# Performance work log

Hardware: AMD Instinct MI355X
Metric: run time of the kernel (lower is better)

Reference implementation:

```python
import jax, jax.numpy as jnp
import numpy as np

IN_DIM = 256
OUT_DIM = 256
HAS_MASK = True


def setup_inputs() -> dict:
    key = jax.random.key(0)
    kx, kq, kk, kv = jax.random.split(key, 4)
    n = 8192
    x = jax.random.normal(kx, (n, IN_DIM), dtype=jnp.float32)
    # parameters (original uses torch.empty; we initialize with small randn)
    scale = 1.0 / np.sqrt(IN_DIM)
    W_query = jax.random.normal(kq, (IN_DIM, OUT_DIM), dtype=jnp.float32) * scale
    W_key = jax.random.normal(kk, (IN_DIM, OUT_DIM), dtype=jnp.float32) * scale
    W_value = jax.random.normal(kv, (IN_DIM, OUT_DIM), dtype=jnp.float32) * scale
    return {"x": x, "W_query": W_query, "W_key": W_key, "W_value": W_value}


def reference(x, W_query, W_key, W_value):
    n = x.shape[0]
    q = x @ W_query            # [n, d]
    k = x @ W_key              # [n, d]
    v = x @ W_value            # [n, d]
    sqrt_d = jnp.sqrt(jnp.asarray(OUT_DIM, dtype=jnp.float32))
    scores = (q @ k.T) / sqrt_d  # [n, n]
    if HAS_MASK:
        # torch.triu(-1e9 * ones(n, n)) keeps the diagonal -> diagonal is masked too
        mask = jnp.triu(jnp.full((n, n), -1000000000.0, dtype=jnp.float32))
        scores = scores + mask
    attn = jax.nn.softmax(scores, axis=1)  # row-wise softmax
    return attn @ v            # [n, d]
```

## Files before the change

### kernel.cpp

```cpp
#include <hip/hip_runtime.h>
#include <hip/hip_bf16.h>
#include <stdint.h>

#define DIM 256

typedef float f32x4  __attribute__((ext_vector_type(4)));
typedef float f32x16 __attribute__((ext_vector_type(16)));
typedef short bf16x8 __attribute__((ext_vector_type(8)));
typedef short bf16x4 __attribute__((ext_vector_type(4)));

__device__ __forceinline__ unsigned short f2bf(float f) {
  union { float f; uint32_t u; } v; v.f = f;
  uint32_t u = v.u;
  u += 0x7FFFu + ((u >> 16) & 1u);
  return (unsigned short)(u >> 16);
}

__device__ __forceinline__ uint32_t pack2(float lo, float hi) {
  return (uint32_t)f2bf(lo) | ((uint32_t)f2bf(hi) << 16);
}

__device__ __forceinline__ void gload16(const unsigned short* g, unsigned short* l) {
  __builtin_amdgcn_global_load_lds(
      (const __attribute__((address_space(1))) unsigned int*)g,
      (__attribute__((address_space(3))) unsigned int*)l, 16, 0, 0);
}

__global__ __launch_bounds__(256) void k_prep(const float* __restrict__ Wq,
    const float* __restrict__ Wk, const float* __restrict__ Wv,
    unsigned short* __restrict__ Wt, const float* __restrict__ x,
    float* __restrict__ partial, int n) {
  __shared__ unsigned short WL32[32][264];
  if (blockIdx.x < 24) {
    const int w  = blockIdx.x >> 3;
    const int kc = blockIdx.x & 7;
    const float* W = (w == 0) ? Wq : (w == 1) ? Wk : Wv;
    const int tid = threadIdx.x;
#pragma unroll
    for (int it = 0; it < 8; ++it) {
      const int row = it * 4 + (tid >> 6);
      const int col = (tid & 63) * 4;
      f32x4 v = *(const f32x4*)(W + (size_t)(kc * 32 + row) * DIM + col);
      bf16x4 b;
      b[0] = (short)f2bf(v[0]); b[1] = (short)f2bf(v[1]);
      b[2] = (short)f2bf(v[2]); b[3] = (short)f2bf(v[3]);
      *(bf16x4*)(&WL32[row][col]) = b;
    }
    __syncthreads();
    const int lane = tid & 63;
    const int ww = tid >> 6;
    const int g = lane >> 4, c = lane & 15;
#pragma unroll
    for (int jt = 0; jt < 4; ++jt) {
      const int nt = jt * 4 + ww;
      bf16x8 o;
#pragma unroll
      for (int j = 0; j < 8; ++j)
        o[j] = (short)WL32[g * 8 + j][nt * 16 + c];
      *(bf16x8*)(Wt + (size_t)((w * 16 + nt) * 8 + kc) * 512 + lane * 8) = o;
    }
  } else {
    const int b = blockIdx.x - 24, tid = threadIdx.x;
    float acc = 0.f;
    const float* xp = x + (size_t)b * 128 * DIM + tid;
    for (int r = 0; r < 128; ++r) acc += xp[r * DIM];
    partial[b * DIM + tid] = acc;
  }
}

__global__ __launch_bounds__(256, 2) void k_proj(const float* __restrict__ x,
    const unsigned short* __restrict__ Wt, unsigned short* __restrict__ Q,
    unsigned short* __restrict__ KS, unsigned short* __restrict__ VS, int n) {
  __shared__ unsigned short XL[64][264];
  __shared__ unsigned short WL[2][16][512];
  const int rb = blockIdx.x * 64;
  const int w = blockIdx.y;
  const int wave = threadIdx.x >> 6;
  const int lane = threadIdx.x & 63;
  const int g = lane >> 4;
  const int c = lane & 15;
  const int row0 = rb + wave * 16;

  for (int rr = 0; rr < 16; ++rr) {
    const int r = wave * 16 + rr;
    f32x4 v = *(const f32x4*)(x + (size_t)(rb + r) * DIM + lane * 4);
    bf16x4 b;
    b[0] = (short)f2bf(v[0]); b[1] = (short)f2bf(v[1]);
    b[2] = (short)f2bf(v[2]); b[3] = (short)f2bf(v[3]);
    *(bf16x4*)(&XL[r][lane * 4]) = b;
  }
  __syncthreads();

  bf16x8 af[8];
#pragma unroll
  for (int kc = 0; kc < 8; ++kc)
    af[kc] = *(const bf16x8*)(&XL[wave * 16 + c][kc * 32 + g * 8]);

  const unsigned short* Wsrc = Wt + (size_t)w * DIM * DIM + lane * 8;
  auto stagew = [&](int buf, int p) {
#pragma unroll
    for (int q2 = 0; q2 < 4; ++q2) {
      const int m = wave * 4 + q2;
      gload16(Wsrc + (size_t)(p * 16 + m) * 512, &WL[buf][m][0]);
    }
  };

  f32x4 acc[16];
#pragma unroll
  for (int t = 0; t < 16; ++t) acc[t] = (f32x4){0.f, 0.f, 0.f, 0.f};

  stagew(0, 0);
  int buf = 0;
#pragma unroll 1
  for (int p = 0; p < 8; ++p) {
    if (p < 7) {
      stagew(buf ^ 1, p + 1);
      asm volatile("s_waitcnt vmcnt(4)" ::: "memory");
    } else {
      asm volatile("s_waitcnt vmcnt(0)" ::: "memory");
    }
    __builtin_amdgcn_sched_barrier(0);
    __builtin_amdgcn_s_barrier();
    __builtin_amdgcn_sched_barrier(0);
#pragma unroll
    for (int q = 0; q < 2; ++q) {
      const int nt = p * 2 + q;
#pragma unroll
      for (int kc = 0; kc < 8; ++kc) {
        bf16x8 b = *(const bf16x8*)(&WL[buf][q * 8 + kc][lane * 8]);
        acc[nt] = __builtin_amdgcn_mfma_f32_16x16x32_bf16(af[kc], b, acc[nt], 0, 0, 0);
      }
    }
    __builtin_amdgcn_sched_barrier(0);
    __builtin_amdgcn_s_barrier();
    __builtin_amdgcn_sched_barrier(0);
    buf ^= 1;
  }

  if (w == 0) {
#pragma unroll
    for (int nt = 0; nt < 16; ++nt)
#pragma unroll
      for (int r = 0; r < 4; ++r)
        Q[(size_t)(row0 + 4 * g + r) * DIM + nt * 16 + c] = f2bf(acc[nt][r] * 0.0625f);
  } else if (w == 1) {
    const int kbase = (row0 >> 5) * 8192 + ((row0 & 31) + 4 * g) * 8 + (c & 7);
#pragma unroll
    for (int nt = 0; nt < 16; ++nt) {
      const int gb = (2 * nt + (c >> 3)) * 256;
#pragma unroll
      for (int r = 0; r < 4; ++r)
        KS[kbase + gb + r * 8] = f2bf(acc[nt][r]);
    }
  } else {
    const int j0 = row0 + 4 * g;
    unsigned short* vdst = VS + (size_t)(j0 >> 5) * 8192
                              + ((j0 >> 3) & 3) * 2048 + (j0 & 7);
#pragma unroll
    for (int nt = 0; nt < 16; ++nt) {
      const int col = nt * 16 + c;
      bf16x4 pv;
      pv[0] = (short)f2bf(acc[nt][0]); pv[1] = (short)f2bf(acc[nt][1]);
      pv[2] = (short)f2bf(acc[nt][2]); pv[3] = (short)f2bf(acc[nt][3]);
      *(bf16x4*)(vdst + col * 8) = pv;
    }
  }
}

__global__ void k_meanB(const float* __restrict__ partial, const float* __restrict__ Wv,
                        float* __restrict__ out, int n) {
  __shared__ float xm[DIM];
  const int tid = threadIdx.x;
  float acc = 0.f;
  const int nb = n / 128;
  for (int b = 0; b < nb; ++b) acc += partial[b * DIM + tid];
  xm[tid] = acc / (float)n;
  __syncthreads();
  float o = 0.f;
  for (int k = 0; k < DIM; ++k) o += xm[k] * Wv[k * DIM + tid];
  out[tid] = o;
}

__global__ __launch_bounds__(512, 4) void k_flash2(const unsigned short* __restrict__ Q,
    const unsigned short* __restrict__ KS, const unsigned short* __restrict__ VS,
    float* __restrict__ out, int n) {
  __shared__ float so[4][16][257];
  __shared__ float sml[4][2][16];
  __shared__ unsigned short plds[8][16][40];

  const int wave = threadIdx.x >> 6;
  const int lane = threadIdx.x & 63;
  const int g = lane >> 4;
  const int c = lane & 15;
  const int ntiles = n >> 4;
  const int tile = ntiles - 1 - (int)blockIdx.x;
  const int qb = tile << 4;

  bf16x8 qf[8];
  const unsigned short* qp = Q + (size_t)(qb + c) * DIM;
#pragma unroll
  for (int kc = 0; kc < 8; ++kc)
    qf[kc] = *(const bf16x8*)(qp + kc * 32 + g * 8);

  f32x4 o[16];
#pragma unroll
  for (int t = 0; t < 16; ++t) o[t] = (f32x4){0.f, 0.f, 0.f, 0.f};
  float m_r[4] = {-1e30f, -1e30f, -1e30f, -1e30f};
  float l_r[4] = {0.f, 0.f, 0.f, 0.f};

  const int nchunk = ((qb + 14) >> 5) + 1;
  for (int kt = wave; kt < nchunk; kt += 8) {
    const int k0 = kt << 5;
    const unsigned short* kch = KS + (size_t)(k0 >> 5) * 8192;
    f32x4 s0 = {0.f, 0.f, 0.f, 0.f}, s1 = {0.f, 0.f, 0.f, 0.f};
#pragma unroll
    for (int kc = 0; kc < 8; ++kc) {
      bf16x8 kb0 = *(const bf16x8*)(kch + (4 * kc + g) * 256 + c * 8);
      bf16x8 kb1 = *(const bf16x8*)(kch + (4 * kc + g) * 256 + (16 + c) * 8);
      s0 = __builtin_amdgcn_mfma_f32_16x16x32_bf16(qf[kc], kb0, s0, 0, 0, 0);
      s1 = __builtin_amdgcn_mfma_f32_16x16x32_bf16(qf[kc], kb1, s1, 0, 0, 0);
    }
    if (k0 + 31 >= qb) {
#pragma unroll
      for (int r = 0; r < 4; ++r) {
        const int qrow = qb + 4 * g + r;
        if (k0 + c >= qrow)      s0[r] = -1e9f;
        if (k0 + 16 + c >= qrow) s1[r] = -1e9f;
      }
    }
    f32x4 p0, p1;
    float alpha[4];
#pragma unroll
    for (int r = 0; r < 4; ++r) {
      float mx = fmaxf(s0[r], s1[r]);
      mx = fmaxf(mx, __shfl_xor(mx, 1, 64));
      mx = fmaxf(mx, __shfl_xor(mx, 2, 64));
      mx = fmaxf(mx, __shfl_xor(mx, 4, 64));
      mx = fmaxf(mx, __shfl_xor(mx, 8, 64));
      const float mn = fmaxf(m_r[r], mx);
      const float a = __expf(m_r[r] - mn);
      p0[r] = __expf(s0[r] - mn);
      p1[r] = __expf(s1[r] - mn);
      float ls = p0[r] + p1[r];
      ls += __shfl_xor(ls, 1, 64);
      ls += __shfl_xor(ls, 2, 64);
      ls += __shfl_xor(ls, 4, 64);
      ls += __shfl_xor(ls, 8, 64);
      l_r[r] = l_r[r] * a + ls;
      m_r[r] = mn;
      alpha[r] = a;
    }
#pragma unroll
    for (int t = 0; t < 16; ++t) {
      o[t][0] *= alpha[0]; o[t][1] *= alpha[1];
      o[t][2] *= alpha[2]; o[t][3] *= alpha[3];
    }
#pragma unroll
    for (int r = 0; r < 4; ++r) {
      plds[wave][4 * g + r][c]      = f2bf(p0[r]);
      plds[wave][4 * g + r][16 + c] = f2bf(p1[r]);
    }
    asm volatile("s_waitcnt lgkmcnt(0)" ::: "memory");
    const bf16x8 pa = *(const bf16x8*)(&plds[wave][c][8 * g]);
    const unsigned short* vch = VS + (size_t)(k0 >> 5) * 8192 + g * 2048;
#pragma unroll
    for (int t = 0; t < 16; ++t) {
      bf16x8 vb = *(const bf16x8*)(vch + (size_t)(c + 16 * t) * 8);
      o[t] = __builtin_amdgcn_mfma_f32_16x16x32_bf16(pa, vb, o[t], 0, 0, 0);
    }
  }

  auto write_slot = [&](int s) {
#pragma unroll
    for (int r = 0; r < 4; ++r) {
      const int row = 4 * g + r;
#pragma unroll
      for (int t = 0; t < 16; ++t) so[s][row][t * 16 + c] = o[t][r];
      if (c == 0) { sml[s][0][row] = m_r[r]; sml[s][1][row] = l_r[r]; }
    }
  };
  auto merge_slot = [&](int s) {
    float aa[4], ab[4];
#pragma unroll
    for (int r = 0; r < 4; ++r) {
      const int row = 4 * g + r;
      const float mb = sml[s][0][row], lb = sml[s][1][row];
      const float ms = fmaxf(m_r[r], mb);
      aa[r] = __expf(m_r[r] - ms);
      ab[r] = __expf(mb - ms);
      l_r[r] = l_r[r] * aa[r] + lb * ab[r];
      m_r[r] = ms;
    }
#pragma unroll
    for (int t = 0; t < 16; ++t)
#pragma unroll
      for (int r = 0; r < 4; ++r)
        o[t][r] = o[t][r] * aa[r] + so[s][4 * g + r][t * 16 + c] * ab[r];
  };

  __syncthreads();
  if (wave >= 4) write_slot(wave - 4);
  __syncthreads();
  if (wave < 4) merge_slot(wave);
  __syncthreads();
  if (wave == 2 || wave == 3) write_slot(wave - 2);
  __syncthreads();
  if (wave < 2) merge_slot(wave);
  __syncthreads();
  if (wave == 1) write_slot(0);
  __syncthreads();
  if (wave == 0) {
    merge_slot(0);
#pragma unroll
    for (int r = 0; r < 4; ++r) {
      const int qrow = qb + 4 * g + r;
      if (qrow == 0) continue;
      const float inv = 1.0f / l_r[r];
#pragma unroll
      for (int t = 0; t < 16; ++t)
        out[(size_t)qrow * DIM + t * 16 + c] = o[t][r] * inv;
    }
  }
}

template <int CH>
__global__ __launch_bounds__(256, 2) void k_flash8(const unsigned short* __restrict__ Q,
    const unsigned short* __restrict__ KS, const unsigned short* __restrict__ VS,
    unsigned short* __restrict__ po, float* __restrict__ pl, int n) {
  __shared__ unsigned short KL[2][32 * 32 * 8];
  __shared__ unsigned short VL[2][4 * 256 * 8];

  const int wave = threadIdx.x >> 6;
  const int lane = threadIdx.x & 63;
  const int r32 = lane & 31;
  const int h   = lane >> 5;

  const int bid = (int)(gridDim.x - 1 - blockIdx.x);
  int t = 0, cacc = 0;
  for (;;) {
    const int ns = (4 * t + 4 + CH - 1) / CH;
    if (cacc + ns > bid) break;
    cacc += ns; ++t;
  }
  const int sp = bid - cacc;
  const int nsplit = (4 * t + 4 + CH - 1) / CH;
  const int qb = t << 7;
  const int qw = qb + (wave << 5);
  const int nch = 4 * t + 4;
  const int qrow_me = qw + r32;

  bf16x8 qf[16];
  const unsigned short* qp = Q + (size_t)qrow_me * DIM + h * 8;
#pragma unroll
  for (int kc = 0; kc < 16; ++kc)
    qf[kc] = *(const bf16x8*)(qp + kc * 16);

  f32x16 o[8];
#pragma unroll
  for (int dt = 0; dt < 8; ++dt)
#pragma unroll
    for (int r = 0; r < 16; ++r) o[dt][r] = 0.f;
  float lac = 0.f;

  const unsigned short* Ksrc = KS + (size_t)lane * 8;
  const unsigned short* Vsrc = VS + (size_t)lane * 8;

  auto stage = [&](int buf, int k0) {
    const size_t cb = (size_t)(k0 >> 5) * 8192;
#pragma unroll
    for (int jj = 0; jj < 4; ++jj)
      gload16(Ksrc + cb + (8 * wave + 2 * jj) * 256,
              &KL[buf][(8 * wave + 2 * jj) * 256]);
#pragma unroll
    for (int jj = 0; jj < 4; ++jj)
      gload16(Vsrc + cb + wave * 2048 + jj * 512,
              &VL[buf][(wave * 256 + jj * 64) * 8]);
  };

  int ci = sp;
  stage(0, ci << 5);
  int buf = 0;
  for (;;) {
    const int k0 = ci << 5;
    const int cin = ci + nsplit;
    const bool more = (cin < nch);
    if (more) {
      stage(buf ^ 1, cin << 5);
      asm volatile("s_waitcnt vmcnt(8)" ::: "memory");
    } else {
      asm volatile("s_waitcnt vmcnt(0)" ::: "memory");
    }
    __builtin_amdgcn_sched_barrier(0);
    __builtin_amdgcn_s_barrier();
    __builtin_amdgcn_sched_barrier(0);

    if (k0 <= qw + 30) {
      f32x16 sa, sb;
#pragma unroll
      for (int r = 0; r < 16; ++r) { sa[r] = 0.f; sb[r] = 0.f; }
      __builtin_amdgcn_s_setprio(1);
#pragma unroll
      for (int kc = 0; kc < 8; ++kc) {
        bf16x8 kbA = *(const bf16x8*)(&KL[buf][((2 * kc + h) * 32 + r32) * 8]);
        bf16x8 kbB = *(const bf16x8*)(&KL[buf][((2 * kc + 16 + h) * 32 + r32) * 8]);
        sa = __builtin_amdgcn_mfma_f32_32x32x16_bf16(kbA, qf[kc], sa, 0, 0, 0);
        sb = __builtin_amdgcn_mfma_f32_32x32x16_bf16(kbB, qf[kc + 8], sb, 0, 0, 0);
      }
      __builtin_amdgcn_s_setprio(0);
      f32x16 s = sa + sb;
      if (k0 + 31 >= qw) {
#pragma unroll
        for (int r = 0; r < 16; ++r) {
          const int key = k0 + (r & 3) + 8 * (r >> 2) + 4 * h;
          if (key >= qrow_me) s[r] = -1e9f;
        }
      }
      uint32_t pk0l, pk0h, pk1l, pk1h, pk2l, pk2h, pk3l, pk3h;
      {
        float p0, p1, p2, p3;
        p0 = __expf(s[0] - 16.f);  p1 = __expf(s[1] - 16.f);
        p2 = __expf(s[2] - 16.f);  p3 = __expf(s[3] - 16.f);
        lac += (p0 + p1) + (p2 + p3);
        pk0l = pack2(p0, p1); pk0h = pack2(p2, p3);
        p0 = __expf(s[4] - 16.f);  p1 = __expf(s[5] - 16.f);
        p2 = __expf(s[6] - 16.f);  p3 = __expf(s[7] - 16.f);
        lac += (p0 + p1) + (p2 + p3);
        pk1l = pack2(p0, p1); pk1h = pack2(p2, p3);
        p0 = __expf(s[8] - 16.f);  p1 = __expf(s[9] - 16.f);
        p2 = __expf(s[10] - 16.f); p3 = __expf(s[11] - 16.f);
        lac += (p0 + p1) + (p2 + p3);
        pk2l = pack2(p0, p1); pk2h = pack2(p2, p3);
        p0 = __expf(s[12] - 16.f); p1 = __expf(s[13] - 16.f);
        p2 = __expf(s[14] - 16.f); p3 = __expf(s[15] - 16.f);
        lac += (p0 + p1) + (p2 + p3);
        pk3l = pack2(p0, p1); pk3h = pack2(p2, p3);
      }
      {
        uint32_t a0 = pk0l, b0 = pk1l, a1 = pk0h, b1 = pk1h;
        asm volatile("v_permlane32_swap_b32 %0, %1" : "+v"(a0), "+v"(b0));
        asm volatile("v_permlane32_swap_b32 %0, %1" : "+v"(a1), "+v"(b1));
        union { bf16x8 v; uint32_t u[4]; } pa;
        pa.u[0] = a0; pa.u[1] = a1; pa.u[2] = b0; pa.u[3] = b1;
        __builtin_amdgcn_s_setprio(1);
#pragma unroll
        for (int dt = 0; dt < 8; ++dt) {
          bf16x8 vb = *(const bf16x8*)(&VL[buf][(h * 256 + dt * 32 + r32) * 8]);
          o[dt] = __builtin_amdgcn_mfma_f32_32x32x16_bf16(pa.v, vb, o[dt], 0, 0, 0);
        }
        __builtin_amdgcn_s_setprio(0);
      }
      {
        uint32_t a0 = pk2l, b0 = pk3l, a1 = pk2h, b1 = pk3h;
        asm volatile("v_permlane32_swap_b32 %0, %1" : "+v"(a0), "+v"(b0));
        asm volatile("v_permlane32_swap_b32 %0, %1" : "+v"(a1), "+v"(b1));
        union { bf16x8 v; uint32_t u[4]; } pa;
        pa.u[0] = a0; pa.u[1] = a1; pa.u[2] = b0; pa.u[3] = b1;
        __builtin_amdgcn_s_setprio(1);
#pragma unroll
        for (int dt = 0; dt < 8; ++dt) {
          bf16x8 vb = *(const bf16x8*)(&VL[buf][((2 + h) * 256 + dt * 32 + r32) * 8]);
          o[dt] = __builtin_amdgcn_mfma_f32_32x32x16_bf16(pa.v, vb, o[dt], 0, 0, 0);
        }
        __builtin_amdgcn_s_setprio(0);
      }
    }

    __builtin_amdgcn_sched_barrier(0);
    __builtin_amdgcn_s_barrier();
    __builtin_amdgcn_sched_barrier(0);
    if (!more) break;
    buf ^= 1;
    ci = cin;
  }

  const float lacF = lac + __shfl_xor(lac, 32, 64);
  unsigned short* pow = po + ((size_t)bid * 128 + (wave << 5)) * DIM;
  float* plw = pl + (size_t)bid * 128 + (wave << 5);
  if (h == 0) plw[r32] = lacF;
#pragma unroll
  for (int r = 0; r < 16; ++r) {
    const int srow = (r & 3) + 8 * (r >> 2) + 4 * h;
#pragma unroll
    for (int dt = 0; dt < 8; ++dt)
      pow[(size_t)srow * DIM + dt * 32 + r32] = f2bf(o[dt][r]);
  }
}

template <int CH>
__global__ __launch_bounds__(256) void k_comb(const unsigned short* __restrict__ po,
    const float* __restrict__ pl, const float* __restrict__ partial,
    const float* __restrict__ Wv, float* __restrict__ out, int n) {
  const int row = blockIdx.x * 16 + (threadIdx.x >> 4);
  const int c0 = (threadIdx.x & 15) * 16;
  const int t = row >> 7;
  int cumt = 0;
  for (int u = 0; u < t; ++u) cumt += (4 * u + 4 + CH - 1) / CH;
  const int ns = (4 * t + 4 + CH - 1) / CH;
  const int lr = row & 127;

  float acc[16];
#pragma unroll
  for (int j = 0; j < 16; ++j) acc[j] = 0.f;
  float lsum = 0.f;
  for (int s = 0; s < ns; ++s) {
    lsum += pl[(size_t)(cumt + s) * 128 + lr];
    const unsigned short* pp = po + ((size_t)(cumt + s) * 128 + lr) * DIM + c0;
    bf16x8 v0 = *(const bf16x8*)(pp);
    bf16x8 v1 = *(const bf16x8*)(pp + 8);
#pragma unroll
    for (int j = 0; j < 8; ++j) {
      union { float f; uint32_t u; } cv0, cv1;
      cv0.u = ((uint32_t)(unsigned short)v0[j]) << 16;
      cv1.u = ((uint32_t)(unsigned short)v1[j]) << 16;
      acc[j]     += cv0.f;
      acc[8 + j] += cv1.f;
    }
  }
  const float inv = (lsum > 0.f) ? 1.0f / lsum : 0.f;
#pragma unroll
  for (int j = 0; j < 16; ++j)
    out[(size_t)row * DIM + c0 + j] = acc[j] * inv;

  if (blockIdx.x == 0) {
    __shared__ float xm[DIM];
    const int tid = threadIdx.x;
    float s = 0.f;
    const int nb = n / 128;
    for (int b = 0; b < nb; ++b) s += partial[b * DIM + tid];
    xm[tid] = s / (float)n;
    __syncthreads();
    float oo = 0.f;
    for (int k = 0; k < DIM; ++k) oo += xm[k] * Wv[k * DIM + tid];
    out[tid] = oo;
  }
}

extern "C" void kernel_launch(void* const* d_in, const int* in_sizes, int n_in,
                              void* d_out, int out_size, void* d_ws, size_t ws_size,
                              hipStream_t stream) {
  const float* x  = (const float*)d_in[0];
  const float* Wq = (const float*)d_in[1];
  const float* Wk = (const float*)d_in[2];
  const float* Wv = (const float*)d_in[3];
  float* out = (float*)d_out;
  const int n = in_sizes[0] / DIM;
  const int T = n >> 7;

  char* ws = (char*)d_ws;
  const size_t wt_bytes  = (size_t)3 * DIM * DIM * 2;
  const size_t mat_bytes = (size_t)n * DIM * 2;
  const size_t par_bytes = (size_t)(n / 128) * DIM * 4;
  const size_t base = wt_bytes + 3 * mat_bytes + par_bytes;

  unsigned short* Wt = (unsigned short*)(ws);
  unsigned short* Q  = (unsigned short*)(ws + wt_bytes);
  unsigned short* KS = (unsigned short*)(ws + wt_bytes + mat_bytes);
  unsigned short* VS = (unsigned short*)(ws + wt_bytes + 2 * mat_bytes);
  float* partial     = (float*)(ws + wt_bytes + 3 * mat_bytes);

  auto slots_for = [&](int CH) {
    int s = 0;
    for (int t = 0; t < T; ++t) s += (4 * t + 4 + CH - 1) / CH;
    return s;
  };
  const int ns18 = slots_for(18);
  const int ns36 = slots_for(36);
  const size_t need18 = base + (size_t)ns18 * 128 * 4 + (size_t)ns18 * 128 * DIM * 2;
  const size_t need36 = base + (size_t)ns36 * 128 * 4 + (size_t)ns36 * 128 * DIM * 2;
  int mode = 0, nslots = 0;
  if (ws_size >= need18)      { mode = 18; nslots = ns18; }
  else if (ws_size >= need36) { mode = 36; nslots = ns36; }
  float* pl          = (float*)(ws + base);
  unsigned short* po = (unsigned short*)(ws + base + (size_t)nslots * 128 * 4);

  hipLaunchKernelGGL(k_prep, dim3(24 + n / 128), dim3(256), 0, stream,
                     Wq, Wk, Wv, Wt, x, partial, n);
  hipLaunchKernelGGL(k_proj, dim3(n / 64, 3), dim3(256), 0, stream, x, Wt, Q, KS, VS, n);
  if (mode == 18) {
    hipLaunchKernelGGL((k_flash8<18>), dim3(nslots), dim3(256), 0, stream,
                       Q, KS, VS, po, pl, n);
    hipLaunchKernelGGL((k_comb<18>), dim3(n / 16), dim3(256), 0, stream,
                       po, pl, partial, Wv, out, n);
  } else if (mode == 36) {
    hipLaunchKernelGGL((k_flash8<36>), dim3(nslots), dim3(256), 0, stream,
                       Q, KS, VS, po, pl, n);
    hipLaunchKernelGGL((k_comb<36>), dim3(n / 16), dim3(256), 0, stream,
                       po, pl, partial, Wv, out, n);
  } else {
    hipLaunchKernelGGL(k_flash2, dim3(n / 16), dim3(512), 0, stream, Q, KS, VS, out, n);
    hipLaunchKernelGGL(k_meanB, dim3(1), dim3(256), 0, stream, partial, Wv, out, n);
  }
}
```

Measured before the change: 102.9 us.

## Double flash query tile to 256 rows with 8 waves; stage projection outputs via LDS

The flash split-K kernel now processes 256 query rows per block with 512 threads (8 waves), so each staged K/V chunk is shared by twice as many waves and each wave issues half the loads. Slot and combine indexing move to 256-row tiles, and the launcher picks the finest split size (9, 13, 18, 27) that fits the workspace. The projection kernel writes its results into shared memory first and then copies them out with coalesced 16-byte stores instead of scattered 2-byte stores. The larger blocks raise per-block resource use and coarsen causal load balancing.

```diff
diff --git a/kernel.cpp b/kernel.cpp
--- a/kernel.cpp
+++ b/kernel.cpp
@@ -71,7 +71,7 @@
 __global__ __launch_bounds__(256, 2) void k_proj(const float* __restrict__ x,
     const unsigned short* __restrict__ Wt, unsigned short* __restrict__ Q,
     unsigned short* __restrict__ KS, unsigned short* __restrict__ VS, int n) {
-  __shared__ unsigned short XL[64][264];
+  __shared__ unsigned short XL[64 * 264];
   __shared__ unsigned short WL[2][16][512];
   const int rb = blockIdx.x * 64;
   const int w = blockIdx.y;
@@ -79,7 +79,6 @@
   const int lane = threadIdx.x & 63;
   const int g = lane >> 4;
   const int c = lane & 15;
-  const int row0 = rb + wave * 16;
 
   for (int rr = 0; rr < 16; ++rr) {
     const int r = wave * 16 + rr;
@@ -87,14 +86,14 @@
     bf16x4 b;
     b[0] = (short)f2bf(v[0]); b[1] = (short)f2bf(v[1]);
     b[2] = (short)f2bf(v[2]); b[3] = (short)f2bf(v[3]);
-    *(bf16x4*)(&XL[r][lane * 4]) = b;
+    *(bf16x4*)(&XL[r * 264 + lane * 4]) = b;
   }
   __syncthreads();
 
   bf16x8 af[8];
 #pragma unroll
   for (int kc = 0; kc < 8; ++kc)
-    af[kc] = *(const bf16x8*)(&XL[wave * 16 + c][kc * 32 + g * 8]);
+    af[kc] = *(const bf16x8*)(&XL[(wave * 16 + c) * 264 + kc * 32 + g * 8]);
 
   const unsigned short* Wsrc = Wt + (size_t)w * DIM * DIM + lane * 8;
   auto stagew = [&](int buf, int p) {
@@ -142,29 +141,38 @@
     for (int nt = 0; nt < 16; ++nt)
 #pragma unroll
       for (int r = 0; r < 4; ++r)
-        Q[(size_t)(row0 + 4 * g + r) * DIM + nt * 16 + c] = f2bf(acc[nt][r] * 0.0625f);
+        XL[(wave * 16 + 4 * g + r) * 256 + nt * 16 + c] = f2bf(acc[nt][r] * 0.0625f);
   } else if (w == 1) {
-    const int kbase = (row0 >> 5) * 8192 + ((row0 & 31) + 4 * g) * 8 + (c & 7);
+    const int lrB = wave * 16 + 4 * g;
 #pragma unroll
     for (int nt = 0; nt < 16; ++nt) {
-      const int gb = (2 * nt + (c >> 3)) * 256;
-#pragma unroll
-      for (int r = 0; r < 4; ++r)
-        KS[kbase + gb + r * 8] = f2bf(acc[nt][r]);
+      const int gran = 2 * nt + (c >> 3);
+#pragma unroll
+      for (int r = 0; r < 4; ++r) {
+        const int lr = lrB + r;
+        XL[(lr >> 5) * 8192 + gran * 256 + (lr & 31) * 8 + (c & 7)] = f2bf(acc[nt][r]);
+      }
     }
   } else {
-    const int j0 = row0 + 4 * g;
-    unsigned short* vdst = VS + (size_t)(j0 >> 5) * 8192
-                              + ((j0 >> 3) & 3) * 2048 + (j0 & 7);
+    const int j0 = wave * 16 + 4 * g;
+    const int vbase = (j0 >> 5) * 8192 + ((j0 >> 3) & 3) * 2048 + (j0 & 7);
 #pragma unroll
     for (int nt = 0; nt < 16; ++nt) {
       const int col = nt * 16 + c;
       bf16x4 pv;
       pv[0] = (short)f2bf(acc[nt][0]); pv[1] = (short)f2bf(acc[nt][1]);
       pv[2] = (short)f2bf(acc[nt][2]); pv[3] = (short)f2bf(acc[nt][3]);
-      *(bf16x4*)(vdst + col * 8) = pv;
-    }
-  }
+      *(bf16x4*)(&XL[vbase + col * 8]) = pv;
+    }
+  }
+  __syncthreads();
+  unsigned short* dstB = (w == 0) ? Q + (size_t)rb * 256
+                       : (w == 1) ? KS + (size_t)(rb >> 5) * 8192
+                                  : VS + (size_t)(rb >> 5) * 8192;
+#pragma unroll
+  for (int it = 0; it < 8; ++it)
+    *(bf16x8*)(dstB + it * 2048 + threadIdx.x * 8) =
+        *(const bf16x8*)(&XL[it * 2048 + threadIdx.x * 8]);
 }
 
 __global__ void k_meanB(const float* __restrict__ partial, const float* __restrict__ Wv,
@@ -324,7 +332,7 @@
 }
 
 template <int CH>
-__global__ __launch_bounds__(256, 2) void k_flash8(const unsigned short* __restrict__ Q,
+__global__ __launch_bounds__(512, 2) void k_flash9(const unsigned short* __restrict__ Q,
     const unsigned short* __restrict__ KS, const unsigned short* __restrict__ VS,
     unsigned short* __restrict__ po, float* __restrict__ pl, int n) {
   __shared__ unsigned short KL[2][32 * 32 * 8];
@@ -338,15 +346,15 @@
   const int bid = (int)(gridDim.x - 1 - blockIdx.x);
   int t = 0, cacc = 0;
   for (;;) {
-    const int ns = (4 * t + 4 + CH - 1) / CH;
+    const int ns = (8 * t + 8 + CH - 1) / CH;
     if (cacc + ns > bid) break;
     cacc += ns; ++t;
   }
   const int sp = bid - cacc;
-  const int nsplit = (4 * t + 4 + CH - 1) / CH;
-  const int qb = t << 7;
+  const int nsplit = (8 * t + 8 + CH - 1) / CH;
+  const int qb = t << 8;
   const int qw = qb + (wave << 5);
-  const int nch = 4 * t + 4;
+  const int nch = 8 * t + 8;
   const int qrow_me = qw + r32;
 
   bf16x8 qf[16];
@@ -368,13 +376,13 @@
   auto stage = [&](int buf, int k0) {
     const size_t cb = (size_t)(k0 >> 5) * 8192;
 #pragma unroll
-    for (int jj = 0; jj < 4; ++jj)
-      gload16(Ksrc + cb + (8 * wave + 2 * jj) * 256,
-              &KL[buf][(8 * wave + 2 * jj) * 256]);
-#pragma unroll
-    for (int jj = 0; jj < 4; ++jj)
-      gload16(Vsrc + cb + wave * 2048 + jj * 512,
-              &VL[buf][(wave * 256 + jj * 64) * 8]);
+    for (int jj = 0; jj < 2; ++jj)
+      gload16(Ksrc + cb + (4 * wave + 2 * jj) * 256,
+              &KL[buf][(4 * wave + 2 * jj) * 256]);
+#pragma unroll
+    for (int jj = 0; jj < 2; ++jj)
+      gload16(Vsrc + cb + (2 * wave + jj) * 512,
+              &VL[buf][(2 * wave + jj) * 512]);
   };
 
   int ci = sp;
@@ -386,7 +394,7 @@
     const bool more = (cin < nch);
     if (more) {
       stage(buf ^ 1, cin << 5);
-      asm volatile("s_waitcnt vmcnt(8)" ::: "memory");
+      asm volatile("s_waitcnt vmcnt(4)" ::: "memory");
     } else {
       asm volatile("s_waitcnt vmcnt(0)" ::: "memory");
     }
@@ -474,8 +482,8 @@
   }
 
   const float lacF = lac + __shfl_xor(lac, 32, 64);
-  unsigned short* pow = po + ((size_t)bid * 128 + (wave << 5)) * DIM;
-  float* plw = pl + (size_t)bid * 128 + (wave << 5);
+  unsigned short* pow = po + ((size_t)bid * 256 + (wave << 5)) * DIM;
+  float* plw = pl + (size_t)bid * 256 + (wave << 5);
   if (h == 0) plw[r32] = lacF;
 #pragma unroll
   for (int r = 0; r < 16; ++r) {
@@ -487,24 +495,24 @@
 }
 
 template <int CH>
-__global__ __launch_bounds__(256) void k_comb(const unsigned short* __restrict__ po,
+__global__ __launch_bounds__(256) void k_comb9(const unsigned short* __restrict__ po,
     const float* __restrict__ pl, const float* __restrict__ partial,
     const float* __restrict__ Wv, float* __restrict__ out, int n) {
   const int row = blockIdx.x * 16 + (threadIdx.x >> 4);
   const int c0 = (threadIdx.x & 15) * 16;
-  const int t = row >> 7;
+  const int t = row >> 8;
   int cumt = 0;
-  for (int u = 0; u < t; ++u) cumt += (4 * u + 4 + CH - 1) / CH;
-  const int ns = (4 * t + 4 + CH - 1) / CH;
-  const int lr = row & 127;
+  for (int u = 0; u < t; ++u) cumt += (8 * u + 8 + CH - 1) / CH;
+  const int ns = (8 * t + 8 + CH - 1) / CH;
+  const int lr = row & 255;
 
   float acc[16];
 #pragma unroll
   for (int j = 0; j < 16; ++j) acc[j] = 0.f;
   float lsum = 0.f;
   for (int s = 0; s < ns; ++s) {
-    lsum += pl[(size_t)(cumt + s) * 128 + lr];
-    const unsigned short* pp = po + ((size_t)(cumt + s) * 128 + lr) * DIM + c0;
+    lsum += pl[(size_t)(cumt + s) * 256 + lr];
+    const unsigned short* pp = po + ((size_t)(cumt + s) * 256 + lr) * DIM + c0;
     bf16x8 v0 = *(const bf16x8*)(pp);
     bf16x8 v1 = *(const bf16x8*)(pp + 8);
 #pragma unroll
@@ -544,7 +552,7 @@
   const float* Wv = (const float*)d_in[3];
   float* out = (float*)d_out;
   const int n = in_sizes[0] / DIM;
-  const int T = n >> 7;
+  const int T = n >> 8;
 
   char* ws = (char*)d_ws;
   const size_t wt_bytes  = (size_t)3 * DIM * DIM * 2;
@@ -560,32 +568,34 @@
 
   auto slots_for = [&](int CH) {
     int s = 0;
-    for (int t = 0; t < T; ++t) s += (4 * t + 4 + CH - 1) / CH;
+    for (int t = 0; t < T; ++t) s += (8 * t + 8 + CH - 1) / CH;
     return s;
   };
-  const int ns18 = slots_for(18);
-  const int ns36 = slots_for(36);
-  const size_t need18 = base + (size_t)ns18 * 128 * 4 + (size_t)ns18 * 128 * DIM * 2;
-  const size_t need36 = base + (size_t)ns36 * 128 * 4 + (size_t)ns36 * 128 * DIM * 2;
+  const int chs[4] = {9, 13, 18, 27};
   int mode = 0, nslots = 0;
-  if (ws_size >= need18)      { mode = 18; nslots = ns18; }
-  else if (ws_size >= need36) { mode = 36; nslots = ns36; }
+  for (int i = 0; i < 4; ++i) {
+    const int nsl = slots_for(chs[i]);
+    const size_t need = base + (size_t)nsl * 256 * 4 + (size_t)nsl * 256 * DIM * 2;
+    if (ws_size >= need) { mode = chs[i]; nslots = nsl; break; }
+  }
   float* pl          = (float*)(ws + base);
-  unsigned short* po = (unsigned short*)(ws + base + (size_t)nslots * 128 * 4);
+  unsigned short* po = (unsigned short*)(ws + base + (size_t)nslots * 256 * 4);
 
   hipLaunchKernelGGL(k_prep, dim3(24 + n / 128), dim3(256), 0, stream,
                      Wq, Wk, Wv, Wt, x, partial, n);
   hipLaunchKernelGGL(k_proj, dim3(n / 64, 3), dim3(256), 0, stream, x, Wt, Q, KS, VS, n);
-  if (mode == 18) {
-    hipLaunchKernelGGL((k_flash8<18>), dim3(nslots), dim3(256), 0, stream,
-                       Q, KS, VS, po, pl, n);
-    hipLaunchKernelGGL((k_comb<18>), dim3(n / 16), dim3(256), 0, stream,
-                       po, pl, partial, Wv, out, n);
-  } else if (mode == 36) {
-    hipLaunchKernelGGL((k_flash8<36>), dim3(nslots), dim3(256), 0, stream,
-                       Q, KS, VS, po, pl, n);
-    hipLaunchKernelGGL((k_comb<36>), dim3(n / 16), dim3(256), 0, stream,
-                       po, pl, partial, Wv, out, n);
+  if (mode == 9) {
+    hipLaunchKernelGGL((k_flash9<9>), dim3(nslots), dim3(512), 0, stream, Q, KS, VS, po, pl, n);
+    hipLaunchKernelGGL((k_comb9<9>), dim3(n / 16), dim3(256), 0, stream, po, pl, partial, Wv, out, n);
+  } else if (mode == 13) {
+    hipLaunchKernelGGL((k_flash9<13>), dim3(nslots), dim3(512), 0, stream, Q, KS, VS, po, pl, n);
+    hipLaunchKernelGGL((k_comb9<13>), dim3(n / 16), dim3(256), 0, stream, po, pl, partial, Wv, out, n);
+  } else if (mode == 18) {
+    hipLaunchKernelGGL((k_flash9<18>), dim3(nslots), dim3(512), 0, stream, Q, KS, VS, po, pl, n);
+    hipLaunchKernelGGL((k_comb9<18>), dim3(n / 16), dim3(256), 0, stream, po, pl, partial, Wv, out, n);
+  } else if (mode == 27) {
+    hipLaunchKernelGGL((k_flash9<27>), dim3(nslots), dim3(512), 0, stream, Q, KS, VS, po, pl, n);
+    hipLaunchKernelGGL((k_comb9<27>), dim3(n / 16), dim3(256), 0, stream, po, pl, partial, Wv, out, n);
   } else {
     hipLaunchKernelGGL(k_flash2, dim3(n / 16), dim3(512), 0, stream, Q, KS, VS, out, n);
     hipLaunchKernelGGL(k_meanB, dim3(1), dim3(256), 0, stream, partial, Wv, out, n);
```

Result: slower. 112.1 us (+9.0%).

## Stage projection outputs in LDS for coalesced 16-byte global stores

Applied to the files above, without the earlier changes.

The projection kernel now writes its Q, K and V results into the reused shared-memory X tile in the final swizzled layout. After a barrier, each block copies the 64x256 tile to global memory with contiguous 16-byte vector stores, replacing scattered 2-byte and 8-byte stores. It also switches pack2 to the hardware v_cvt_pk_bf16_f32 instruction. This costs an extra barrier and LDS traffic, and the LDS writes may hit bank conflicts.

```diff
diff --git a/kernel.cpp b/kernel.cpp
--- a/kernel.cpp
+++ b/kernel.cpp
@@ -17,7 +17,9 @@
 }
 
 __device__ __forceinline__ uint32_t pack2(float lo, float hi) {
-  return (uint32_t)f2bf(lo) | ((uint32_t)f2bf(hi) << 16);
+  uint32_t r;
+  asm("v_cvt_pk_bf16_f32 %0, %1, %2" : "=v"(r) : "v"(lo), "v"(hi));
+  return r;
 }
 
 __device__ __forceinline__ void gload16(const unsigned short* g, unsigned short* l) {
@@ -71,7 +73,7 @@
 __global__ __launch_bounds__(256, 2) void k_proj(const float* __restrict__ x,
     const unsigned short* __restrict__ Wt, unsigned short* __restrict__ Q,
     unsigned short* __restrict__ KS, unsigned short* __restrict__ VS, int n) {
-  __shared__ unsigned short XL[64][264];
+  __shared__ unsigned short XL[64 * 264];
   __shared__ unsigned short WL[2][16][512];
   const int rb = blockIdx.x * 64;
   const int w = blockIdx.y;
@@ -79,7 +81,6 @@
   const int lane = threadIdx.x & 63;
   const int g = lane >> 4;
   const int c = lane & 15;
-  const int row0 = rb + wave * 16;
 
   for (int rr = 0; rr < 16; ++rr) {
     const int r = wave * 16 + rr;
@@ -87,14 +88,14 @@
     bf16x4 b;
     b[0] = (short)f2bf(v[0]); b[1] = (short)f2bf(v[1]);
     b[2] = (short)f2bf(v[2]); b[3] = (short)f2bf(v[3]);
-    *(bf16x4*)(&XL[r][lane * 4]) = b;
+    *(bf16x4*)(&XL[r * 264 + lane * 4]) = b;
   }
   __syncthreads();
 
   bf16x8 af[8];
 #pragma unroll
   for (int kc = 0; kc < 8; ++kc)
-    af[kc] = *(const bf16x8*)(&XL[wave * 16 + c][kc * 32 + g * 8]);
+    af[kc] = *(const bf16x8*)(&XL[(wave * 16 + c) * 264 + kc * 32 + g * 8]);
 
   const unsigned short* Wsrc = Wt + (size_t)w * DIM * DIM + lane * 8;
   auto stagew = [&](int buf, int p) {
@@ -142,29 +143,38 @@
     for (int nt = 0; nt < 16; ++nt)
 #pragma unroll
       for (int r = 0; r < 4; ++r)
-        Q[(size_t)(row0 + 4 * g + r) * DIM + nt * 16 + c] = f2bf(acc[nt][r] * 0.0625f);
+        XL[(wave * 16 + 4 * g + r) * 256 + nt * 16 + c] = f2bf(acc[nt][r] * 0.0625f);
   } else if (w == 1) {
-    const int kbase = (row0 >> 5) * 8192 + ((row0 & 31) + 4 * g) * 8 + (c & 7);
+    const int lrB = wave * 16 + 4 * g;
 #pragma unroll
     for (int nt = 0; nt < 16; ++nt) {
-      const int gb = (2 * nt + (c >> 3)) * 256;
-#pragma unroll
-      for (int r = 0; r < 4; ++r)
-        KS[kbase + gb + r * 8] = f2bf(acc[nt][r]);
+      const int gran = 2 * nt + (c >> 3);
+#pragma unroll
+      for (int r = 0; r < 4; ++r) {
+        const int lr = lrB + r;
+        XL[(lr >> 5) * 8192 + gran * 256 + (lr & 31) * 8 + (c & 7)] = f2bf(acc[nt][r]);
+      }
     }
   } else {
-    const int j0 = row0 + 4 * g;
-    unsigned short* vdst = VS + (size_t)(j0 >> 5) * 8192
-                              + ((j0 >> 3) & 3) * 2048 + (j0 & 7);
+    const int j0 = wave * 16 + 4 * g;
+    const int vbase = (j0 >> 5) * 8192 + ((j0 >> 3) & 3) * 2048 + (j0 & 7);
 #pragma unroll
     for (int nt = 0; nt < 16; ++nt) {
       const int col = nt * 16 + c;
       bf16x4 pv;
       pv[0] = (short)f2bf(acc[nt][0]); pv[1] = (short)f2bf(acc[nt][1]);
       pv[2] = (short)f2bf(acc[nt][2]); pv[3] = (short)f2bf(acc[nt][3]);
-      *(bf16x4*)(vdst + col * 8) = pv;
-    }
-  }
+      *(bf16x4*)(&XL[vbase + col * 8]) = pv;
+    }
+  }
+  __syncthreads();
+  unsigned short* dstB = (w == 0) ? Q + (size_t)rb * 256
+                       : (w == 1) ? KS + (size_t)(rb >> 5) * 8192
+                                  : VS + (size_t)(rb >> 5) * 8192;
+#pragma unroll
+  for (int it = 0; it < 8; ++it)
+    *(bf16x8*)(dstB + it * 2048 + threadIdx.x * 8) =
+        *(const bf16x8*)(&XL[it * 2048 + threadIdx.x * 8]);
 }
 
 __global__ void k_meanB(const float* __restrict__ partial, const float* __restrict__ Wv,
```

Result: no change. 101.7 us (-1.2%).
